# Kernel optimization log

Measured on AMD Instinct MI355X. Metric: run time of the kernel, lower is better.

Reference implementation:

```python
import jax, jax.numpy as jnp
import numpy as np

OUT_DIM = 64
N_NODES = 50000
N_EDGES = 1000000


def setup_inputs() -> dict:
    key = jax.random.key(0)
    k1, k2, k3, k4, k5, k6 = jax.random.split(key, 6)
    return {
        "G_h": jax.random.normal(k1, (N_NODES, OUT_DIM), dtype=jnp.float32),
        "K_h": jax.random.normal(k2, (N_NODES, OUT_DIM), dtype=jnp.float32),
        "Q_h": jax.random.normal(k3, (N_NODES, OUT_DIM), dtype=jnp.float32),
        "V_h": jax.random.normal(k4, (N_NODES, 1, OUT_DIM), dtype=jnp.float32),
        "src": jax.random.randint(k5, (N_EDGES,), 0, N_NODES, dtype=jnp.int64),
        "dst": jax.random.randint(k6, (N_EDGES,), 0, N_NODES, dtype=jnp.int64),
    }


def reference(G_h, K_h, Q_h, V_h, src, dst):
    inv_sqrt_d = 1.0 / np.sqrt(OUT_DIM).astype(np.float32)
    # edge-wise gather of node features
    diff = G_h[src] - G_h[dst]                                   # [E, D]
    dist = -jnp.sqrt(jnp.sum(diff * diff, axis=-1) + 1e-6)       # [E]
    distance = jnp.exp(jnp.clip(dist * inv_sqrt_d, -5.0, 5.0))   # [E]
    score = jnp.sum(K_h[src] * Q_h[dst], axis=-1)                # [E]
    score_e = jnp.exp(jnp.clip(score * inv_sqrt_d, -5.0, 5.0))   # [E]
    weight = (score_e * distance)[:, None, None]                 # [E,1,1]
    v1_h = weight * V_h[src]                                     # [E,1,D]
    return v1_h
```

## Files before the change

### kernel.cpp

```cpp
#include <hip/hip_runtime.h>
#include <math.h>

typedef float f32x4 __attribute__((ext_vector_type(4)));

#define MAXNB 256
#define BSHIFT 8
#define UNROLL 8


__global__ void zero_kernel(int* p, int n) {
    int i = blockIdx.x * blockDim.x + threadIdx.x;
    if (i < n) p[i] = 0;
}

__global__ __launch_bounds__(256) void hist_kernel(
    const int* __restrict__ src, int nE, int nb, int* __restrict__ counts)
{
    __shared__ int lc[MAXNB];
    for (int i = threadIdx.x; i < nb; i += blockDim.x) lc[i] = 0;
    __syncthreads();
    for (int e = blockIdx.x * blockDim.x + threadIdx.x; e < nE;
         e += gridDim.x * blockDim.x)
        atomicAdd(&lc[src[e] >> BSHIFT], 1);
    __syncthreads();
    for (int i = threadIdx.x; i < nb; i += blockDim.x) {
        int c = lc[i];
        if (c) atomicAdd(&counts[i], c);
    }
}

__global__ __launch_bounds__(256) void scan_kernel(
    const int* __restrict__ counts, int nb, int* __restrict__ cursor)
{
    __shared__ int buf[MAXNB];
    int t = threadIdx.x;
    int v = (t < nb) ? counts[t] : 0;
    buf[t] = v;
    __syncthreads();
    #pragma unroll
    for (int off = 1; off < MAXNB; off <<= 1) {
        int x = (t >= off) ? buf[t - off] : 0;
        __syncthreads();
        buf[t] += x;
        __syncthreads();
    }
    if (t < nb) cursor[t] = buf[t] - v;
}

__global__ __launch_bounds__(256) void scatter_kernel(
    const int* __restrict__ src, const int* __restrict__ dst, int nE, int nb,
    int* __restrict__ cursor, int2* __restrict__ eidx)
{
    __shared__ int lc[MAXNB];
    __shared__ int lb[MAXNB];
    const int chunkSize = blockDim.x * UNROLL;
    for (int chunk = blockIdx.x * chunkSize; chunk < nE;
         chunk += gridDim.x * chunkSize) {
        for (int i = threadIdx.x; i < nb; i += blockDim.x) lc[i] = 0;
        __syncthreads();
        int myb[UNROLL], myoff[UNROLL], pack[UNROLL];
        #pragma unroll
        for (int u = 0; u < UNROLL; u++) {
            int e = chunk + u * blockDim.x + threadIdx.x;
            if (e < nE) {
                int s = src[e];
                pack[u] = s | (dst[e] << 16);
                myb[u] = s >> BSHIFT;
                myoff[u] = atomicAdd(&lc[myb[u]], 1);
            } else myb[u] = -1;
        }
        __syncthreads();
        for (int i = threadIdx.x; i < nb; i += blockDim.x) {
            int c = lc[i];
            lb[i] = c ? atomicAdd(&cursor[i], c) : 0;
        }
        __syncthreads();
        #pragma unroll
        for (int u = 0; u < UNROLL; u++) {
            if (myb[u] >= 0) {
                int pos = lb[myb[u]] + myoff[u];
                int e = chunk + u * blockDim.x + threadIdx.x;
                eidx[pos] = make_int2(pack[u], e);
            }
        }
        __syncthreads();
    }
}

__global__ __launch_bounds__(256) void edge_message_kernel(
    const float* __restrict__ G,
    const float* __restrict__ K,
    const float* __restrict__ Q,
    const float* __restrict__ V,
    const int2* __restrict__ eidx,
    float* __restrict__ out,
    int nE)
{
    const int tid  = threadIdx.x;
    const int slot = tid >> 4;
    const int sub  = tid & 15;

    const int nx = gridDim.x >> 3;
    const int chunkIdx = (blockIdx.x & 7) * nx + (blockIdx.x >> 3);
    const int perBlock = (nE + gridDim.x - 1) / gridDim.x;
    const int start = chunkIdx * perBlock;
    const int end   = min(start + perBlock, nE);

    const f32x4* __restrict__ G4 = (const f32x4*)G;
    const f32x4* __restrict__ K4 = (const f32x4*)K;
    const f32x4* __restrict__ Q4 = (const f32x4*)Q;
    const f32x4* __restrict__ V4 = (const f32x4*)V;
    f32x4* __restrict__ out4 = (f32x4*)out;

    const float inv_sqrt_d = 0.125f;

    for (int i0 = start; i0 < end; i0 += 16) {
        const int i = i0 + slot;
        const bool valid = (i < end);
        const int ic = valid ? i : (end - 1);

        const int2 rec = eidx[ic];
        const unsigned u = (unsigned)rec.x;
        const int s = (int)(u & 0xFFFFu);
        const int d = (int)(u >> 16);
        const int o = rec.y;

        const f32x4 gs = G4[s * 16 + sub];
        const f32x4 gd = G4[d * 16 + sub];
        const f32x4 ks = K4[s * 16 + sub];
        const f32x4 qd = Q4[d * 16 + sub];
        const f32x4 vs = V4[s * 16 + sub];

        const f32x4 df = gs - gd;
        const f32x4 kq = ks * qd;
        float a = df.x * df.x + df.y * df.y + df.z * df.z + df.w * df.w;
        float b = kq.x + kq.y + kq.z + kq.w;

        #pragma unroll
        for (int off = 8; off > 0; off >>= 1) {
            a += __shfl_xor(a, off, 64);
            b += __shfl_xor(b, off, 64);
        }

        float t1 = -sqrtf(a + 1e-6f) * inv_sqrt_d;
        t1 = fminf(fmaxf(t1, -5.0f), 5.0f);
        float t2 = b * inv_sqrt_d;
        t2 = fminf(fmaxf(t2, -5.0f), 5.0f);
        const float w = __expf(t1 + t2);

        if (valid) {
            __builtin_nontemporal_store(w * vs, &out4[(size_t)o * 16 + sub]);
        }
    }
}

extern "C" void kernel_launch(void* const* d_in, const int* in_sizes, int n_in,
                              void* d_out, int out_size, void* d_ws, size_t ws_size,
                              hipStream_t stream)
{
    const float* G   = (const float*)d_in[0];
    const float* K   = (const float*)d_in[1];
    const float* Q   = (const float*)d_in[2];
    const float* V   = (const float*)d_in[3];
    const int*   src = (const int*)d_in[4];
    const int*   dst = (const int*)d_in[5];
    float* out = (float*)d_out;

    const int nE = in_sizes[4];
    const int nNodes = in_sizes[0] / 64;
    const int nb = (nNodes + ((1 << BSHIFT) - 1)) >> BSHIFT;

    int* counts = (int*)d_ws;
    int* cursor = counts + 256;
    int2* eidx  = (int2*)(counts + 512);

    zero_kernel<<<2, 256, 0, stream>>>(counts, 512);
    hist_kernel<<<256, 256, 0, stream>>>(src, nE, nb, counts);
    scan_kernel<<<1, 256, 0, stream>>>(counts, nb, cursor);
    {
        const int chunk = 256 * UNROLL;
        int grid = (nE + chunk - 1) / chunk;
        scatter_kernel<<<grid, 256, 0, stream>>>(src, dst, nE, nb, cursor, eidx);
    }
    {
        int grid = 2048;
        edge_message_kernel<<<grid, 256, 0, stream>>>(G, K, Q, V, eidx, out, nE);
    }
}
```

Baseline: 433.0 us.

## Bucket edges by coarse src group and dst block for 2D gather locality

Changes the edge reordering key from src>>8 to a composite of src>>12 and dst>>8, giving about 3k buckets instead of about 200. Edges in the message kernel are then grouped by both source and destination node ranges, so both the src-side and dst-side feature gathers should hit in cache more often. In exchange the histogram and scatter kernels zero and flush far larger shared-memory tables per block, with many more global cursor atomics, and the scan becomes a serial per-thread pass over 16 entries.

```diff
diff --git a/kernel.cpp b/kernel.cpp
--- a/kernel.cpp
+++ b/kernel.cpp
@@ -3,8 +3,9 @@
 
 typedef float f32x4 __attribute__((ext_vector_type(4)));
 
-#define MAXNB 256
-#define BSHIFT 8
+#define SGSHIFT 12
+#define DBSHIFT 8
+#define MAXKEY 4096
 #define UNROLL 8
 
 
@@ -14,71 +15,85 @@
 }
 
 __global__ __launch_bounds__(256) void hist_kernel(
-    const int* __restrict__ src, int nE, int nb, int* __restrict__ counts)
-{
-    __shared__ int lc[MAXNB];
-    for (int i = threadIdx.x; i < nb; i += blockDim.x) lc[i] = 0;
+    const int* __restrict__ src, const int* __restrict__ dst, int nE, int nkey,
+    int* __restrict__ counts)
+{
+    __shared__ int lc[MAXKEY];
+    for (int i = threadIdx.x; i < nkey; i += blockDim.x) lc[i] = 0;
     __syncthreads();
     for (int e = blockIdx.x * blockDim.x + threadIdx.x; e < nE;
-         e += gridDim.x * blockDim.x)
-        atomicAdd(&lc[src[e] >> BSHIFT], 1);
+         e += gridDim.x * blockDim.x) {
+        int key = ((src[e] >> SGSHIFT) << 8) | (dst[e] >> DBSHIFT);
+        atomicAdd(&lc[key], 1);
+    }
     __syncthreads();
-    for (int i = threadIdx.x; i < nb; i += blockDim.x) {
+    for (int i = threadIdx.x; i < nkey; i += blockDim.x) {
         int c = lc[i];
         if (c) atomicAdd(&counts[i], c);
     }
 }
 
 __global__ __launch_bounds__(256) void scan_kernel(
-    const int* __restrict__ counts, int nb, int* __restrict__ cursor)
-{
-    __shared__ int buf[MAXNB];
-    int t = threadIdx.x;
-    int v = (t < nb) ? counts[t] : 0;
-    buf[t] = v;
+    const int* __restrict__ counts, int nkey, int* __restrict__ cursor)
+{
+    __shared__ int buf[256];
+    const int t = threadIdx.x;
+    const int per = (MAXKEY / 256);
+    int s = 0;
+    #pragma unroll
+    for (int j = 0; j < per; j++) {
+        int idx = t * per + j;
+        if (idx < nkey) s += counts[idx];
+    }
+    buf[t] = s;
     __syncthreads();
     #pragma unroll
-    for (int off = 1; off < MAXNB; off <<= 1) {
+    for (int off = 1; off < 256; off <<= 1) {
         int x = (t >= off) ? buf[t - off] : 0;
         __syncthreads();
         buf[t] += x;
         __syncthreads();
     }
-    if (t < nb) cursor[t] = buf[t] - v;
+    int running = buf[t] - s;
+    #pragma unroll
+    for (int j = 0; j < per; j++) {
+        int idx = t * per + j;
+        if (idx < nkey) { cursor[idx] = running; running += counts[idx]; }
+    }
 }
 
 __global__ __launch_bounds__(256) void scatter_kernel(
-    const int* __restrict__ src, const int* __restrict__ dst, int nE, int nb,
+    const int* __restrict__ src, const int* __restrict__ dst, int nE, int nkey,
     int* __restrict__ cursor, int2* __restrict__ eidx)
 {
-    __shared__ int lc[MAXNB];
-    __shared__ int lb[MAXNB];
+    __shared__ int lc[MAXKEY];
+    __shared__ int lb[MAXKEY];
     const int chunkSize = blockDim.x * UNROLL;
     for (int chunk = blockIdx.x * chunkSize; chunk < nE;
          chunk += gridDim.x * chunkSize) {
-        for (int i = threadIdx.x; i < nb; i += blockDim.x) lc[i] = 0;
-        __syncthreads();
-        int myb[UNROLL], myoff[UNROLL], pack[UNROLL];
+        for (int i = threadIdx.x; i < nkey; i += blockDim.x) lc[i] = 0;
+        __syncthreads();
+        int myk[UNROLL], myoff[UNROLL], pack[UNROLL];
         #pragma unroll
         for (int u = 0; u < UNROLL; u++) {
             int e = chunk + u * blockDim.x + threadIdx.x;
             if (e < nE) {
-                int s = src[e];
-                pack[u] = s | (dst[e] << 16);
-                myb[u] = s >> BSHIFT;
-                myoff[u] = atomicAdd(&lc[myb[u]], 1);
-            } else myb[u] = -1;
-        }
-        __syncthreads();
-        for (int i = threadIdx.x; i < nb; i += blockDim.x) {
+                int s = src[e], d = dst[e];
+                pack[u] = s | (d << 16);
+                myk[u] = ((s >> SGSHIFT) << 8) | (d >> DBSHIFT);
+                myoff[u] = atomicAdd(&lc[myk[u]], 1);
+            } else myk[u] = -1;
+        }
+        __syncthreads();
+        for (int i = threadIdx.x; i < nkey; i += blockDim.x) {
             int c = lc[i];
             lb[i] = c ? atomicAdd(&cursor[i], c) : 0;
         }
         __syncthreads();
         #pragma unroll
         for (int u = 0; u < UNROLL; u++) {
-            if (myb[u] >= 0) {
-                int pos = lb[myb[u]] + myoff[u];
+            if (myk[u] >= 0) {
+                int pos = lb[myk[u]] + myoff[u];
                 int e = chunk + u * blockDim.x + threadIdx.x;
                 eidx[pos] = make_int2(pack[u], e);
             }
@@ -168,19 +183,19 @@
 
     const int nE = in_sizes[4];
     const int nNodes = in_sizes[0] / 64;
-    const int nb = (nNodes + ((1 << BSHIFT) - 1)) >> BSHIFT;
+    const int nkey = ((((nNodes - 1) >> SGSHIFT) + 1) << 8);
 
     int* counts = (int*)d_ws;
-    int* cursor = counts + 256;
-    int2* eidx  = (int2*)(counts + 512);
-
-    zero_kernel<<<2, 256, 0, stream>>>(counts, 512);
-    hist_kernel<<<256, 256, 0, stream>>>(src, nE, nb, counts);
-    scan_kernel<<<1, 256, 0, stream>>>(counts, nb, cursor);
+    int* cursor = counts + MAXKEY;
+    int2* eidx  = (int2*)(counts + 2 * MAXKEY);
+
+    zero_kernel<<<(nkey + 255) / 256, 256, 0, stream>>>(counts, nkey);
+    hist_kernel<<<256, 256, 0, stream>>>(src, dst, nE, nkey, counts);
+    scan_kernel<<<1, 256, 0, stream>>>(counts, nkey, cursor);
     {
         const int chunk = 256 * UNROLL;
         int grid = (nE + chunk - 1) / chunk;
-        scatter_kernel<<<grid, 256, 0, stream>>>(src, dst, nE, nb, cursor, eidx);
+        scatter_kernel<<<grid, 256, 0, stream>>>(src, dst, nE, nkey, cursor, eidx);
     }
     {
         int grid = 2048;
```

Measured after the change: 460.2 us. 6.3% more time.
